# Performance work log

Measured on AMD Instinct MI355X. Metric: run time of the kernel, lower is better.

Reference implementation:

```python
import jax, jax.numpy as jnp
import numpy as np

N_NODES = 100000
N_EDGES = 1600000
IN_C = 128
HID_C = 128
OUT_C = 64
N_GRAPHS = 64


def setup_inputs() -> dict:
    key = jax.random.key(0)
    ks = jax.random.split(key, 12)
    x = jax.random.normal(ks[0], (N_NODES, IN_C), dtype=jnp.float32)
    edge_index = jax.random.randint(ks[1], (2, N_EDGES), 0, N_NODES, dtype=jnp.int64)
    batch = jnp.sort(jax.random.randint(ks[2], (N_NODES,), 0, N_GRAPHS, dtype=jnp.int64))
    def glorot(k, fan_in, fan_out):
        s = jnp.sqrt(6.0 / (fan_in + fan_out))
        return jax.random.uniform(k, (fan_in, fan_out), jnp.float32, -s, s)
    W1 = glorot(ks[3], IN_C, HID_C);  b1 = jnp.zeros((HID_C,), jnp.float32)
    W2 = glorot(ks[4], HID_C, HID_C); b2 = jnp.zeros((HID_C,), jnp.float32)
    W3 = glorot(ks[5], HID_C, HID_C); b3 = jnp.zeros((HID_C,), jnp.float32)
    Wlin = glorot(ks[6], HID_C, OUT_C)
    blin = jnp.zeros((OUT_C,), jnp.float32)
    return {"x": x, "edge_index": edge_index, "batch": batch,
            "W1": W1, "b1": b1, "W2": W2, "b2": b2, "W3": W3, "b3": b3,
            "Wlin": Wlin, "blin": blin}


def _gcn_conv(x, W, b, src, dst, norm):
    # PyG GCNConv: h = x @ W; out[dst] += norm * h[src]; out += b
    h = x @ W
    msg = h[src] * norm[:, None]                     # [E+N, C] edge-wise gather (memory-bound)
    out = jax.ops.segment_sum(msg, dst, num_segments=N_NODES)
    return out + b


def reference(x, edge_index, batch, W1, b1, W2, b2, W3, b3, Wlin, blin):
    # add self-loops (PyG default add_self_loops=True)
    loops = jnp.arange(N_NODES, dtype=edge_index.dtype)
    src = jnp.concatenate([edge_index[0], loops])
    dst = jnp.concatenate([edge_index[1], loops])
    # symmetric normalization: deg over dst with unit edge weights
    deg = jax.ops.segment_sum(jnp.ones_like(src, dtype=x.dtype), dst, num_segments=N_NODES)
    dinv = jnp.where(deg > 0, jax.lax.rsqrt(deg), 0.0)
    norm = dinv[src] * dinv[dst]                     # [E+N]

    h = jax.nn.relu(_gcn_conv(x, W1, b1, src, dst, norm))
    h = jax.nn.relu(_gcn_conv(h, W2, b2, src, dst, norm))
    h = jax.nn.relu(_gcn_conv(h, W3, b3, src, dst, norm))

    # global mean pool over graphs
    sums = jax.ops.segment_sum(h, batch, num_segments=N_GRAPHS)
    cnts = jax.ops.segment_sum(jnp.ones((N_NODES,), h.dtype), batch, num_segments=N_GRAPHS)
    pooled = sums / jnp.clip(cnts, 1.0)[:, None]     # [G, HID_C]
    return pooled @ Wlin + blin                      # [G, OUT_C]
```

## Files before the change

### kernel.cpp

```cpp
#include <hip/hip_runtime.h>
#include <stdint.h>

#define C_HID 128
#define NGRAPH 64
#define COUT 64
#define NBLK 256
#define BKT 256
#define NBUK_MAX 512
#define SCAN_CH 4096

typedef short bf16x8 __attribute__((ext_vector_type(8)));
typedef float f32x4 __attribute__((ext_vector_type(4)));
typedef float f32x2 __attribute__((ext_vector_type(2)));

__device__ __forceinline__ unsigned short f2bf(float f){
  unsigned int u = __builtin_bit_cast(unsigned int, f);
  u = u + 0x7FFFu + ((u >> 16) & 1u);
  return (unsigned short)(u >> 16);
}
__device__ __forceinline__ int clampi(int v, int lo, int hi){
  return v < lo ? lo : (v > hi ? hi : v);
}

__global__ void k_zero(float* __restrict__ out, int n){
  int i = blockIdx.x*blockDim.x + threadIdx.x;
  if (i < n) out[i] = 0.f;
}

__global__ __launch_bounds__(256) void k_cnt(const int* __restrict__ dst,
                                             int* __restrict__ cntg,
                                             int E, int N, int NBUK, int chunk){
  __shared__ int cnt[NBUK_MAX];
  int blk = blockIdx.x, t = threadIdx.x;
  for (int b = t; b < NBUK; b += 256) cnt[b] = 0;
  __syncthreads();
  int e0 = blk*chunk, e1 = min(E, e0 + chunk);
  for (int e = e0 + t; e < e1; e += 256)
    atomicAdd(&cnt[clampi(dst[e], 0, N-1) >> 8], 1);
  __syncthreads();
  for (int b = t; b < NBUK; b += 256)
    cntg[b*NBLK + blk] = cnt[b];
}

__global__ __launch_bounds__(256) void k_scanA(const int* __restrict__ cnt,
                                               int* __restrict__ bsum, int n){
  __shared__ int red[256];
  int blk = blockIdx.x, t = threadIdx.x;
  int base = blk*SCAN_CH + t*16;
  int s = 0;
  #pragma unroll
  for (int j = 0; j < 16; ++j){ int i = base + j; s += (i < n) ? cnt[i] : 0; }
  red[t] = s; __syncthreads();
  for (int off = 128; off > 0; off >>= 1){
    if (t < off) red[t] += red[t + off];
    __syncthreads();
  }
  if (t == 0) bsum[blk] = red[0];
}

__global__ __launch_bounds__(256) void k_scanB(const int* __restrict__ bsum,
                                               int* __restrict__ bbase,
                                               int* __restrict__ bases, int nb, int n){
  __shared__ int buf[256];
  int t = threadIdx.x;
  int v = (t < nb) ? bsum[t] : 0;
  buf[t] = v; __syncthreads();
  for (int off = 1; off < 256; off <<= 1){
    int add = (t >= off) ? buf[t-off] : 0;
    __syncthreads();
    buf[t] += add;
    __syncthreads();
  }
  if (t < nb) bbase[t] = buf[t] - v;
  if (t == nb-1) bases[n] = buf[t];
}

__global__ __launch_bounds__(256) void k_scanC(const int* __restrict__ cnt,
                                               const int* __restrict__ bbase,
                                               int* __restrict__ bases, int n){
  __shared__ int buf[256];
  int blk = blockIdx.x, t = threadIdx.x;
  int base = blk*SCAN_CH + t*16;
  int loc[16]; int s = 0;
  #pragma unroll
  for (int j = 0; j < 16; ++j){ int i = base + j; loc[j] = (i < n) ? cnt[i] : 0; s += loc[j]; }
  buf[t] = s; __syncthreads();
  for (int off = 1; off < 256; off <<= 1){
    int add = (t >= off) ? buf[t-off] : 0;
    __syncthreads();
    buf[t] += add;
    __syncthreads();
  }
  int run = bbase[blk] + buf[t] - s;
  #pragma unroll
  for (int j = 0; j < 16; ++j){
    int i = base + j;
    if (i < n) bases[i] = run;
    run += loc[j];
  }
}

__global__ __launch_bounds__(256) void k_scat(const int* __restrict__ src,
                                              const int* __restrict__ dst,
                                              const int* __restrict__ bases,
                                              unsigned int* __restrict__ rec,
                                              int E, int N, int NBUK, int chunk){
  __shared__ int cur[NBUK_MAX];
  int blk = blockIdx.x, t = threadIdx.x;
  for (int b = t; b < NBUK; b += 256) cur[b] = bases[b*NBLK + blk];
  __syncthreads();
  int e0 = blk*chunk, e1 = min(E, e0 + chunk);
  for (int e = e0 + t; e < e1; e += 256){
    int d = clampi(dst[e], 0, N-1);
    int s = clampi(src[e], 0, N-1);
    int p = atomicAdd(&cur[d >> 8], 1);
    rec[p] = (unsigned int)s | ((unsigned int)(d & 255) << 24);
  }
}

__global__ __launch_bounds__(256) void k_csr(const unsigned int* __restrict__ rec,
                                             const int* __restrict__ bases,
                                             int* __restrict__ offs, float* __restrict__ dinv,
                                             int* __restrict__ meta, int E, int N, int NBUK){
  __shared__ int cnt[BKT], loff[BKT], cur[BKT];
  int b = blockIdx.x, t = threadIdx.x;
  cnt[t] = 0;
  __syncthreads();
  int r0 = bases[b*NBLK];
  int r1 = (b+1 < NBUK) ? bases[(b+1)*NBLK] : E;
  for (int i = r0 + t; i < r1; i += 256)
    atomicAdd(&cnt[rec[i] >> 24], 1);
  __syncthreads();
  loff[t] = cnt[t];
  __syncthreads();
  for (int off = 1; off < BKT; off <<= 1){
    int add = (t >= off) ? loff[t - off] : 0;
    __syncthreads();
    loff[t] += add;
    __syncthreads();
  }
  int excl = loff[t] - cnt[t];
  cur[t] = r0 + excl;
  int node = b*BKT + t;
  if (node < N){
    offs[node] = r0 + excl;
    dinv[node] = rsqrtf((float)(cnt[t] + 1));
  }
  if (b == NBUK-1 && t == 0) offs[N] = E;
  __syncthreads();
  for (int i = r0 + t; i < r1; i += 256){
    unsigned int r = rec[i];
    int p = atomicAdd(&cur[r >> 24], 1);
    meta[p] = (int)(r & 0x00FFFFFFu);
  }
}

__global__ void k_xcast(const float2* __restrict__ x, const float* __restrict__ dinv,
                        unsigned short* __restrict__ y, unsigned short* __restrict__ y2, int N){
  int i = blockIdx.x*256 + threadIdx.x;
  int tot = N*64;
  if (i < tot){
    float2 v = x[i];
    float dn = dinv[i >> 6] * 64.f;
    int p = __builtin_amdgcn_cvt_pk_fp8_f32(v.x*dn, v.y*dn, 0, false);
    y[i] = (unsigned short)(p & 0xFFFF);
  } else if (i < tot + 64){
    y[i] = 0;
    y2[i] = 0;
  }
}

__global__ void k_prep(const float* __restrict__ W1, const float* __restrict__ W2,
                       const float* __restrict__ W3, unsigned short* __restrict__ Wt,
                       float* __restrict__ gsum){
  int idx = blockIdx.x*256 + threadIdx.x;
  if (idx < NGRAPH*C_HID) gsum[idx] = 0.f;
  int w = idx >> 14;
  int r = idx & 16383;
  int n = r & 127, k = r >> 7;
  const float* W = (w == 0) ? W1 : (w == 1) ? W2 : W3;
  Wt[(size_t)w*16384 + (size_t)n*128 + k] = f2bf(W[k*128 + n]);
}

__global__ __launch_bounds__(256) void k_spmm(const unsigned short* __restrict__ y,
                       const int* __restrict__ offs,
                       const float* __restrict__ dinv,
                       const int* __restrict__ meta,
                       unsigned int* __restrict__ agg, int N){
  int wv   = __builtin_amdgcn_readfirstlane(threadIdx.x >> 6);
  int lane = threadIdx.x & 63;
  int g = lane >> 3, c = lane & 7;
  int node0 = blockIdx.x*32 + wv*8;
  if (node0 >= N) return;

  int e[9];
  #pragma unroll
  for (int i = 0; i < 9; ++i) e[i] = offs[min(node0 + i, N)];
  int cn[8]; int maxc = 0;
  #pragma unroll
  for (int i = 0; i < 8; ++i){ cn[i] = e[i+1] - e[i]; maxc = max(maxc, cn[i]); }

  int e0l = e[0], cntl = cn[0];
  #pragma unroll
  for (int i = 1; i < 8; ++i){
    e0l  = (g == i) ? e[i]  : e0l;
    cntl = (g == i) ? cn[i] : cntl;
  }
  int nodeg = node0 + g;
  bool nok = nodeg < N;
  int nself = nok ? nodeg : N;

  const uint4* yrow = (const uint4*)y;

  int mv0 = (c      < cntl) ? meta[e0l + c]      : N;
  int mv1 = (c +  8 < cntl) ? meta[e0l + c +  8] : N;
  int mv2 = (c + 16 < cntl) ? meta[e0l + c + 16] : N;
  int mv3 = (c + 24 < cntl) ? meta[e0l + c + 24] : N;
  uint4 us = yrow[(size_t)nself*8 + c];
  float dl = dinv[nok ? nodeg : 0];

  f32x2 acc[8];
  { f32x2 f;
    f = __builtin_amdgcn_cvt_pk_f32_fp8((int)us.x, false); acc[0] = f;
    f = __builtin_amdgcn_cvt_pk_f32_fp8((int)us.x, true);  acc[1] = f;
    f = __builtin_amdgcn_cvt_pk_f32_fp8((int)us.y, false); acc[2] = f;
    f = __builtin_amdgcn_cvt_pk_f32_fp8((int)us.y, true);  acc[3] = f;
    f = __builtin_amdgcn_cvt_pk_f32_fp8((int)us.z, false); acc[4] = f;
    f = __builtin_amdgcn_cvt_pk_f32_fp8((int)us.z, true);  acc[5] = f;
    f = __builtin_amdgcn_cvt_pk_f32_fp8((int)us.w, false); acc[6] = f;
    f = __builtin_amdgcn_cvt_pk_f32_fp8((int)us.w, true);  acc[7] = f; }

  uint4 u[8];
#define SWZ(MV, J) __builtin_amdgcn_ds_swizzle(MV, (0x18 | (((J)&7)<<5)))
#define GA(K, SM) u[K] = yrow[(size_t)(unsigned)(SM)*8 + c]
#define CONV8() do{ _Pragma("unroll") \
  for (int k2 = 0; k2 < 8; ++k2){ \
    f32x2 f; \
    f = __builtin_amdgcn_cvt_pk_f32_fp8((int)u[k2].x, false); acc[0] += f; \
    f = __builtin_amdgcn_cvt_pk_f32_fp8((int)u[k2].x, true);  acc[1] += f; \
    f = __builtin_amdgcn_cvt_pk_f32_fp8((int)u[k2].y, false); acc[2] += f; \
    f = __builtin_amdgcn_cvt_pk_f32_fp8((int)u[k2].y, true);  acc[3] += f; \
    f = __builtin_amdgcn_cvt_pk_f32_fp8((int)u[k2].z, false); acc[4] += f; \
    f = __builtin_amdgcn_cvt_pk_f32_fp8((int)u[k2].z, true);  acc[5] += f; \
    f = __builtin_amdgcn_cvt_pk_f32_fp8((int)u[k2].w, false); acc[6] += f; \
    f = __builtin_amdgcn_cvt_pk_f32_fp8((int)u[k2].w, true);  acc[7] += f; } }while(0)

  if (0 < maxc){
    GA(0,SWZ(mv0,0)); GA(1,SWZ(mv0,1)); GA(2,SWZ(mv0,2)); GA(3,SWZ(mv0,3));
    GA(4,SWZ(mv0,4)); GA(5,SWZ(mv0,5)); GA(6,SWZ(mv0,6)); GA(7,SWZ(mv0,7));
    __builtin_amdgcn_sched_barrier(0);
    CONV8();
  }
  if (8 < maxc){
    GA(0,SWZ(mv1,0)); GA(1,SWZ(mv1,1)); GA(2,SWZ(mv1,2)); GA(3,SWZ(mv1,3));
    GA(4,SWZ(mv1,4)); GA(5,SWZ(mv1,5)); GA(6,SWZ(mv1,6)); GA(7,SWZ(mv1,7));
    __builtin_amdgcn_sched_barrier(0);
    CONV8();
  }
  if (16 < maxc){
    GA(0,SWZ(mv2,0)); GA(1,SWZ(mv2,1)); GA(2,SWZ(mv2,2)); GA(3,SWZ(mv2,3));
    GA(4,SWZ(mv2,4)); GA(5,SWZ(mv2,5)); GA(6,SWZ(mv2,6)); GA(7,SWZ(mv2,7));
    __builtin_amdgcn_sched_barrier(0);
    CONV8();
  }
  if (24 < maxc){
    GA(0,SWZ(mv3,0)); GA(1,SWZ(mv3,1)); GA(2,SWZ(mv3,2)); GA(3,SWZ(mv3,3));
    GA(4,SWZ(mv3,4)); GA(5,SWZ(mv3,5)); GA(6,SWZ(mv3,6)); GA(7,SWZ(mv3,7));
    __builtin_amdgcn_sched_barrier(0);
    CONV8();
  }
#undef SWZ
#undef GA
#undef CONV8

  for (int j = 32; j < maxc; ++j){
    int sm = (j < cntl) ? meta[e0l + j] : N;
    uint4 t = yrow[(size_t)(unsigned)sm*8 + c];
    f32x2 f;
    f = __builtin_amdgcn_cvt_pk_f32_fp8((int)t.x, false); acc[0] += f;
    f = __builtin_amdgcn_cvt_pk_f32_fp8((int)t.x, true);  acc[1] += f;
    f = __builtin_amdgcn_cvt_pk_f32_fp8((int)t.y, false); acc[2] += f;
    f = __builtin_amdgcn_cvt_pk_f32_fp8((int)t.y, true);  acc[3] += f;
    f = __builtin_amdgcn_cvt_pk_f32_fp8((int)t.z, false); acc[4] += f;
    f = __builtin_amdgcn_cvt_pk_f32_fp8((int)t.z, true);  acc[5] += f;
    f = __builtin_amdgcn_cvt_pk_f32_fp8((int)t.w, false); acc[6] += f;
    f = __builtin_amdgcn_cvt_pk_f32_fp8((int)t.w, true);  acc[7] += f;
  }

  float dn = dl * 0.015625f;
  if (nok){
    uint4 w0, w1;
    w0.x = (unsigned int)f2bf(acc[0].x*dn) | ((unsigned int)f2bf(acc[0].y*dn) << 16);
    w0.y = (unsigned int)f2bf(acc[1].x*dn) | ((unsigned int)f2bf(acc[1].y*dn) << 16);
    w0.z = (unsigned int)f2bf(acc[2].x*dn) | ((unsigned int)f2bf(acc[2].y*dn) << 16);
    w0.w = (unsigned int)f2bf(acc[3].x*dn) | ((unsigned int)f2bf(acc[3].y*dn) << 16);
    w1.x = (unsigned int)f2bf(acc[4].x*dn) | ((unsigned int)f2bf(acc[4].y*dn) << 16);
    w1.y = (unsigned int)f2bf(acc[5].x*dn) | ((unsigned int)f2bf(acc[5].y*dn) << 16);
    w1.z = (unsigned int)f2bf(acc[6].x*dn) | ((unsigned int)f2bf(acc[6].y*dn) << 16);
    w1.w = (unsigned int)f2bf(acc[7].x*dn) | ((unsigned int)f2bf(acc[7].y*dn) << 16);
    *(uint4*)(agg + (size_t)nodeg*64 + c*8)     = w0;
    *(uint4*)(agg + (size_t)nodeg*64 + c*8 + 4) = w1;
  }
}

#define GEMM_BLOCKS 512
template<bool FP8OUT, bool POOL>
__global__ __launch_bounds__(256) void k_gemm(const unsigned short* __restrict__ A,
                                              const unsigned short* __restrict__ Wt,
                                              const float* __restrict__ bias,
                                              const float* __restrict__ scale,
                                              void* __restrict__ outv,
                                              const int* __restrict__ batch,
                                              float* __restrict__ gsum, int M){
  __shared__ unsigned short wt[128*136];
  __shared__ float gbuf[2][C_HID];
  {
    const uint4* wsrc = (const uint4*)Wt;
    for (int i = threadIdx.x; i < 4096; i += 256){
      uint4 v = wsrc[i];
      int n = i >> 4, kblk = i & 15;
      *(uint4*)&wt[n*136 + kblk*8] = v;
    }
  }
  __syncthreads();

  int wv = threadIdx.x >> 6, lane = threadIdx.x & 63;
  int q = lane >> 4, ln = lane & 15;
  int tiles = (M + 63) >> 6;

  for (int tile = blockIdx.x; tile < tiles; tile += GEMM_BLOCKS){
    int m0 = tile*64 + wv*16;
    int arow = m0 + ln;
    bool arow_ok = (arow < M);
    int arow_s = arow_ok ? arow : 0;

    f32x4 zero = {0.f, 0.f, 0.f, 0.f};
    f32x4 acc[8];
    #pragma unroll
    for (int t = 0; t < 8; ++t) acc[t] = zero;

    #pragma unroll
    for (int kk = 0; kk < 4; ++kk){
      bf16x8 a;
      if (arow_ok){
        __builtin_memcpy(&a, A + (size_t)arow_s*128 + kk*32 + q*8, 16);
      } else {
        a = (bf16x8){0,0,0,0,0,0,0,0};
      }
      #pragma unroll
      for (int t = 0; t < 8; ++t){
        bf16x8 b;
        __builtin_memcpy(&b, &wt[(t*16 + ln)*136 + kk*32 + q*8], 16);
        acc[t] = __builtin_amdgcn_mfma_f32_16x16x32_bf16(a, b, acc[t], 0, 0, 0);
      }
    }

    if (POOL){
      int tb = tile*64;
      int gA = batch[tb];
      int gB = batch[min(tb + 63, M - 1)];
      bool multi = (gB > gA + 1);
      __syncthreads();
      ((float*)gbuf)[threadIdx.x] = 0.f;
      __syncthreads();
      #pragma unroll
      for (int t = 0; t < 8; ++t){
        float bv = bias[t*16 + ln];
        int ch = t*16 + ln;
        float s0 = 0.f, s1 = 0.f;
        #pragma unroll
        for (int r = 0; r < 4; ++r){
          int row = m0 + q*4 + r;
          if (row < M){
            float v = acc[t][r] + bv;
            v = v > 0.f ? v : 0.f;
            if (multi){
              atomicAdd(&gsum[(size_t)batch[row]*C_HID + ch], v);
            } else if (gB > gA && batch[row] != gA){
              s1 += v;
            } else {
              s0 += v;
            }
          }
        }
        if (!multi){
          if (s0 != 0.f) atomicAdd(&gbuf[0][ch], s0);
          if (s1 != 0.f) atomicAdd(&gbuf[1][ch], s1);
        }
      }
      __syncthreads();
      if (!multi){
        int sel = threadIdx.x >> 7, ch2 = threadIdx.x & 127;
        if (sel == 0 || gB > gA){
          float v = ((float*)gbuf)[threadIdx.x];
          if (v != 0.f)
            atomicAdd(&gsum[(size_t)((sel == 0) ? gA : gB)*C_HID + ch2], v);
        }
      }
    } else {
      float sc[4];
      #pragma unroll
      for (int r = 0; r < 4; ++r){
        int row = m0 + q*4 + r;
        sc[r] = (FP8OUT && row < M) ? scale[row] * 64.f : 1.0f;
      }
      #pragma unroll
      for (int t = 0; t < 8; ++t){
        float bv = bias[t*16 + ln];
        #pragma unroll
        for (int r = 0; r < 4; ++r){
          int row = m0 + q*4 + r;
          if (row < M){
            float v = acc[t][r] + bv;
            v = v > 0.f ? v : 0.f;
            if (FP8OUT){
              v *= sc[r];
              int p = __builtin_amdgcn_cvt_pk_fp8_f32(v, v, 0, false);
              ((unsigned char*)outv)[(size_t)row*128 + t*16 + ln] = (unsigned char)(p & 0xFF);
            } else {
              ((unsigned short*)outv)[(size_t)row*128 + t*16 + ln] = f2bf(v);
            }
          }
        }
      }
    }
  }
}

__device__ __forceinline__ int lower_bound_i(const int* arr, int n, int val){
  int lo = 0, hi = n;
  while (lo < hi){ int mid = (lo + hi) >> 1; if (arr[mid] < val) lo = mid + 1; else hi = mid; }
  return lo;
}

__global__ void k_fin(const float* __restrict__ gsum, const int* __restrict__ batch,
                      const float* __restrict__ Wl, const float* __restrict__ bl,
                      float* __restrict__ out, int N){
  __shared__ float srow[C_HID];
  int g = blockIdx.x, t = threadIdx.x;
  srow[t] = gsum[(size_t)g*C_HID + t];
  __syncthreads();
  if (t < COUT){
    int rs = clampi(lower_bound_i(batch, N, g), 0, N);
    int re = clampi(lower_bound_i(batch, N, g + 1), rs, N);
    float inv = 1.0f / fmaxf((float)(re - rs), 1.0f);
    float o = 0.f;
    for (int k = 0; k < 128; ++k)
      o += srow[k] * Wl[k*COUT + t];
    out[g*COUT + t] = o * inv + bl[t];
  }
}

extern "C" void kernel_launch(void* const* d_in, const int* in_sizes, int n_in,
                              void* d_out, int out_size, void* d_ws, size_t ws_size,
                              hipStream_t stream){
  const float* x0 = (const float*)d_in[0];
  const int* ei   = (const int*)d_in[1];
  const int* batch= (const int*)d_in[2];
  const float* W1 = (const float*)d_in[3];
  const float* b1 = (const float*)d_in[4];
  const float* W2 = (const float*)d_in[5];
  const float* b2 = (const float*)d_in[6];
  const float* W3 = (const float*)d_in[7];
  const float* b3 = (const float*)d_in[8];
  const float* Wl = (const float*)d_in[9];
  const float* bl = (const float*)d_in[10];
  float* out = (float*)d_out;

  int E = in_sizes[1] / 2;
  int N = in_sizes[2];
  const int* src = ei;
  const int* dst = ei + E;
  int NBUK = (N + BKT - 1) / BKT;
  int chunk = (E + NBLK - 1) / NBLK;
  int ncnt = NBUK * NBLK;
  int nsb  = (ncnt + SCAN_CH - 1) / SCAN_CH;

  size_t off_acc = 0;
  auto carve = [&](size_t bytes)->size_t{
    size_t r = off_acc; off_acc += (bytes + 255) & ~(size_t)255; return r;
  };
  size_t o_cnt   = carve((size_t)ncnt*4);
  size_t o_bases = carve((size_t)(ncnt+1)*4);
  size_t o_bsum  = carve(256*4);
  size_t o_bbase = carve(256*4);
  size_t o_offs  = carve((size_t)(N+1)*4);
  size_t o_dinv  = carve((size_t)N*4);
  size_t o_meta  = carve((size_t)E*4);
  size_t o_rec   = carve((size_t)E*4);
  size_t o_yA    = carve((size_t)(N+1)*C_HID);
  size_t o_yB    = carve((size_t)(N+1)*C_HID);
  size_t o_aggb  = carve((size_t)N*C_HID*2);
  size_t o_wt    = carve((size_t)3*128*128*2);
  size_t o_gsum  = carve((size_t)NGRAPH*C_HID*4);
  size_t need = off_acc;

  if (ws_size < need || NBUK > NBUK_MAX || nsb > 256){
    k_zero<<<(out_size+255)/256, 256, 0, stream>>>(out, out_size);
    return;
  }

  char* base = (char*)d_ws;
  int* cntg  = (int*)(base + o_cnt);
  int* bases = (int*)(base + o_bases);
  int* bsum  = (int*)(base + o_bsum);
  int* bbase = (int*)(base + o_bbase);
  int* offs  = (int*)(base + o_offs);
  float* dinv= (float*)(base + o_dinv);
  int* meta  = (int*)(base + o_meta);
  unsigned int* rec   = (unsigned int*)(base + o_rec);
  unsigned short* yA  = (unsigned short*)(base + o_yA);
  unsigned short* yB  = (unsigned short*)(base + o_yB);
  unsigned int* aggb  = (unsigned int*)(base + o_aggb);
  unsigned short* wt  = (unsigned short*)(base + o_wt);
  float* gsum         = (float*)(base + o_gsum);

  k_cnt  <<<NBLK, 256, 0, stream>>>(dst, cntg, E, N, NBUK, chunk);
  k_scanA<<<nsb, 256, 0, stream>>>(cntg, bsum, ncnt);
  k_scanB<<<1, 256, 0, stream>>>(bsum, bbase, bases, nsb, ncnt);
  k_scanC<<<nsb, 256, 0, stream>>>(cntg, bbase, bases, ncnt);
  k_scat <<<NBLK, 256, 0, stream>>>(src, dst, bases, rec, E, N, NBUK, chunk);
  k_csr  <<<NBUK, BKT, 0, stream>>>(rec, bases, offs, dinv, meta, E, N, NBUK);

  k_xcast<<<(N*64 + 64 + 255)/256, 256, 0, stream>>>((const float2*)x0, dinv, yA, yB, N);
  k_prep <<<192, 256, 0, stream>>>(W1, W2, W3, wt, gsum);

  int spmm_grid = (N + 31) / 32;

  k_spmm<<<spmm_grid, 256, 0, stream>>>(yA, offs, dinv, meta, aggb, N);
  k_gemm<true , false><<<GEMM_BLOCKS, 256, 0, stream>>>((const unsigned short*)aggb, wt,           b1, dinv, (void*)yB, nullptr, nullptr, N);
  k_spmm<<<spmm_grid, 256, 0, stream>>>(yB, offs, dinv, meta, aggb, N);
  k_gemm<true , false><<<GEMM_BLOCKS, 256, 0, stream>>>((const unsigned short*)aggb, wt + 16384,   b2, dinv, (void*)yA, nullptr, nullptr, N);
  k_spmm<<<spmm_grid, 256, 0, stream>>>(yA, offs, dinv, meta, aggb, N);
  k_gemm<false, true ><<<GEMM_BLOCKS, 256, 0, stream>>>((const unsigned short*)aggb, wt + 2*16384, b3, dinv, nullptr,    batch,   gsum,    N);

  k_fin<<<NGRAPH, 128, 0, stream>>>(gsum, batch, Wl, bl, out, N);
}
```

Before: 333.0 us.

## Cut kernel launches by fusing scans, prep kernels and final pooling

Replaces the three-kernel per-block prefix scan with global per-bucket atomic counts, scanned by the last-finishing block of k_cnt. k_scat then recounts its chunk locally and reserves ranges with global atomics. k_xcast and k_prep are merged, and the final linear layer runs in the last block of the pooling GEMM. This removes several small launches and their serialization gaps. In exchange, edge order inside a bucket now depends on atomic ordering, k_scat reads dst twice, and the last-block epilogue runs serially on one block.

Result: slower. 498.9 us (+49.8%).

```diff
diff --git a/kernel.cpp b/kernel.cpp
--- a/kernel.cpp
+++ b/kernel.cpp
@@ -7,8 +7,6 @@
 #define NBLK 256
 #define BKT 256
 #define NBUK_MAX 512
-#define SCAN_CH 4096
-
 typedef short bf16x8 __attribute__((ext_vector_type(8)));
 typedef float f32x4 __attribute__((ext_vector_type(4)));
 typedef float f32x2 __attribute__((ext_vector_type(2)));
@@ -28,92 +26,74 @@
 }
 
 __global__ __launch_bounds__(256) void k_cnt(const int* __restrict__ dst,
-                                             int* __restrict__ cntg,
+                                             int* __restrict__ bcnt,
+                                             int* __restrict__ done1,
+                                             int* __restrict__ bases,
+                                             int* __restrict__ cur,
                                              int E, int N, int NBUK, int chunk){
   __shared__ int cnt[NBUK_MAX];
-  int blk = blockIdx.x, t = threadIdx.x;
+  __shared__ int amLast;
+  int t = threadIdx.x;
   for (int b = t; b < NBUK; b += 256) cnt[b] = 0;
   __syncthreads();
-  int e0 = blk*chunk, e1 = min(E, e0 + chunk);
+  int e0 = blockIdx.x*chunk, e1 = min(E, e0 + chunk);
   for (int e = e0 + t; e < e1; e += 256)
     atomicAdd(&cnt[clampi(dst[e], 0, N-1) >> 8], 1);
   __syncthreads();
   for (int b = t; b < NBUK; b += 256)
-    cntg[b*NBLK + blk] = cnt[b];
-}
-
-__global__ __launch_bounds__(256) void k_scanA(const int* __restrict__ cnt,
-                                               int* __restrict__ bsum, int n){
-  __shared__ int red[256];
-  int blk = blockIdx.x, t = threadIdx.x;
-  int base = blk*SCAN_CH + t*16;
-  int s = 0;
-  #pragma unroll
-  for (int j = 0; j < 16; ++j){ int i = base + j; s += (i < n) ? cnt[i] : 0; }
-  red[t] = s; __syncthreads();
-  for (int off = 128; off > 0; off >>= 1){
-    if (t < off) red[t] += red[t + off];
+    if (cnt[b]) atomicAdd(&bcnt[b], cnt[b]);
+  __threadfence();
+  if (t == 0){
+    int old = __hip_atomic_fetch_add(done1, 1, __ATOMIC_ACQ_REL, __HIP_MEMORY_SCOPE_AGENT);
+    amLast = (old == (int)gridDim.x - 1);
+  }
+  __syncthreads();
+  if (!amLast) return;
+
+  __shared__ int sb[512];
+  int a0 = __hip_atomic_load(&bcnt[t],       __ATOMIC_RELAXED, __HIP_MEMORY_SCOPE_AGENT);
+  int a1 = __hip_atomic_load(&bcnt[t + 256], __ATOMIC_RELAXED, __HIP_MEMORY_SCOPE_AGENT);
+  sb[t] = a0; sb[t + 256] = a1;
+  __syncthreads();
+  for (int off = 1; off < 256; off <<= 1){
+    int x0 = (t >= off) ? sb[t - off] : 0;
+    int x1 = (t >= off) ? sb[256 + t - off] : 0;
     __syncthreads();
-  }
-  if (t == 0) bsum[blk] = red[0];
-}
-
-__global__ __launch_bounds__(256) void k_scanB(const int* __restrict__ bsum,
-                                               int* __restrict__ bbase,
-                                               int* __restrict__ bases, int nb, int n){
-  __shared__ int buf[256];
-  int t = threadIdx.x;
-  int v = (t < nb) ? bsum[t] : 0;
-  buf[t] = v; __syncthreads();
-  for (int off = 1; off < 256; off <<= 1){
-    int add = (t >= off) ? buf[t-off] : 0;
+    sb[t] += x0; sb[256 + t] += x1;
     __syncthreads();
-    buf[t] += add;
-    __syncthreads();
-  }
-  if (t < nb) bbase[t] = buf[t] - v;
-  if (t == nb-1) bases[n] = buf[t];
-}
-
-__global__ __launch_bounds__(256) void k_scanC(const int* __restrict__ cnt,
-                                               const int* __restrict__ bbase,
-                                               int* __restrict__ bases, int n){
-  __shared__ int buf[256];
-  int blk = blockIdx.x, t = threadIdx.x;
-  int base = blk*SCAN_CH + t*16;
-  int loc[16]; int s = 0;
-  #pragma unroll
-  for (int j = 0; j < 16; ++j){ int i = base + j; loc[j] = (i < n) ? cnt[i] : 0; s += loc[j]; }
-  buf[t] = s; __syncthreads();
-  for (int off = 1; off < 256; off <<= 1){
-    int add = (t >= off) ? buf[t-off] : 0;
-    __syncthreads();
-    buf[t] += add;
-    __syncthreads();
-  }
-  int run = bbase[blk] + buf[t] - s;
-  #pragma unroll
-  for (int j = 0; j < 16; ++j){
-    int i = base + j;
-    if (i < n) bases[i] = run;
-    run += loc[j];
-  }
+  }
+  int lowTot = sb[255];
+  sb[256 + t] += lowTot;
+  __syncthreads();
+  bases[t]       = sb[t] - a0;        cur[t]       = sb[t] - a0;
+  bases[t + 256] = sb[t + 256] - a1;  cur[t + 256] = sb[t + 256] - a1;
+  if (t == 255) bases[512] = sb[511];
 }
 
 __global__ __launch_bounds__(256) void k_scat(const int* __restrict__ src,
                                               const int* __restrict__ dst,
-                                              const int* __restrict__ bases,
+                                              int* __restrict__ cur,
                                               unsigned int* __restrict__ rec,
                                               int E, int N, int NBUK, int chunk){
-  __shared__ int cur[NBUK_MAX];
-  int blk = blockIdx.x, t = threadIdx.x;
-  for (int b = t; b < NBUK; b += 256) cur[b] = bases[b*NBLK + blk];
-  __syncthreads();
-  int e0 = blk*chunk, e1 = min(E, e0 + chunk);
+  __shared__ int cnt[NBUK_MAX];
+  __shared__ int lbase[NBUK_MAX];
+  int t = threadIdx.x;
+  for (int b = t; b < NBUK; b += 256) cnt[b] = 0;
+  __syncthreads();
+  int e0 = blockIdx.x*chunk, e1 = min(E, e0 + chunk);
+  for (int e = e0 + t; e < e1; e += 256)
+    atomicAdd(&cnt[clampi(dst[e], 0, N-1) >> 8], 1);
+  __syncthreads();
+  for (int b = t; b < NBUK; b += 256)
+    lbase[b] = cnt[b] ? atomicAdd(&cur[b], cnt[b]) : 0;
+  __syncthreads();
+  for (int b = t; b < NBUK; b += 256) cnt[b] = 0;
+  __syncthreads();
   for (int e = e0 + t; e < e1; e += 256){
     int d = clampi(dst[e], 0, N-1);
     int s = clampi(src[e], 0, N-1);
-    int p = atomicAdd(&cur[d >> 8], 1);
+    int b = d >> 8;
+    int p = lbase[b] + atomicAdd(&cnt[b], 1);
     rec[p] = (unsigned int)s | ((unsigned int)(d & 255) << 24);
   }
 }
@@ -126,8 +106,8 @@
   int b = blockIdx.x, t = threadIdx.x;
   cnt[t] = 0;
   __syncthreads();
-  int r0 = bases[b*NBLK];
-  int r1 = (b+1 < NBUK) ? bases[(b+1)*NBLK] : E;
+  int r0 = bases[b];
+  int r1 = bases[b + 1];
   for (int i = r0 + t; i < r1; i += 256)
     atomicAdd(&cnt[rec[i] >> 24], 1);
   __syncthreads();
@@ -155,8 +135,11 @@
   }
 }
 
-__global__ void k_xcast(const float2* __restrict__ x, const float* __restrict__ dinv,
-                        unsigned short* __restrict__ y, unsigned short* __restrict__ y2, int N){
+__global__ void k_prepx(const float2* __restrict__ x, const float* __restrict__ dinv,
+                        unsigned short* __restrict__ y, unsigned short* __restrict__ y2,
+                        const float* __restrict__ W1, const float* __restrict__ W2,
+                        const float* __restrict__ W3, unsigned short* __restrict__ Wt,
+                        float* __restrict__ gsum, int* __restrict__ done3, int N){
   int i = blockIdx.x*256 + threadIdx.x;
   int tot = N*64;
   if (i < tot){
@@ -168,18 +151,15 @@
     y[i] = 0;
     y2[i] = 0;
   }
-}
-
-__global__ void k_prep(const float* __restrict__ W1, const float* __restrict__ W2,
-                       const float* __restrict__ W3, unsigned short* __restrict__ Wt,
-                       float* __restrict__ gsum){
-  int idx = blockIdx.x*256 + threadIdx.x;
-  if (idx < NGRAPH*C_HID) gsum[idx] = 0.f;
-  int w = idx >> 14;
-  int r = idx & 16383;
-  int n = r & 127, k = r >> 7;
-  const float* W = (w == 0) ? W1 : (w == 1) ? W2 : W3;
-  Wt[(size_t)w*16384 + (size_t)n*128 + k] = f2bf(W[k*128 + n]);
+  if (i < 3*16384){
+    int w = i >> 14;
+    int r = i & 16383;
+    int n = r & 127, k = r >> 7;
+    const float* W = (w == 0) ? W1 : (w == 1) ? W2 : W3;
+    Wt[(size_t)w*16384 + (size_t)n*128 + k] = f2bf(W[k*128 + n]);
+  }
+  if (i < NGRAPH*C_HID) gsum[i] = 0.f;
+  if (i == 0) *done3 = 0;
 }
 
 __global__ __launch_bounds__(256) void k_spmm(const unsigned short* __restrict__ y,
@@ -303,6 +283,12 @@
   }
 }
 
+__device__ __forceinline__ int lower_bound_i(const int* arr, int n, int val){
+  int lo = 0, hi = n;
+  while (lo < hi){ int mid = (lo + hi) >> 1; if (arr[mid] < val) lo = mid + 1; else hi = mid; }
+  return lo;
+}
+
 #define GEMM_BLOCKS 512
 template<bool FP8OUT, bool POOL>
 __global__ __launch_bounds__(256) void k_gemm(const unsigned short* __restrict__ A,
@@ -311,9 +297,14 @@
                                               const float* __restrict__ scale,
                                               void* __restrict__ outv,
                                               const int* __restrict__ batch,
-                                              float* __restrict__ gsum, int M){
+                                              float* __restrict__ gsum,
+                                              int* __restrict__ done3,
+                                              const float* __restrict__ Wl,
+                                              const float* __restrict__ bl,
+                                              float* __restrict__ fout, int M){
   __shared__ unsigned short wt[128*136];
   __shared__ float gbuf[2][C_HID];
+  __shared__ int amLast;
   {
     const uint4* wsrc = (const uint4*)Wt;
     for (int i = threadIdx.x; i < 4096; i += 256){
@@ -425,29 +416,30 @@
       }
     }
   }
-}
-
-__device__ __forceinline__ int lower_bound_i(const int* arr, int n, int val){
-  int lo = 0, hi = n;
-  while (lo < hi){ int mid = (lo + hi) >> 1; if (arr[mid] < val) lo = mid + 1; else hi = mid; }
-  return lo;
-}
-
-__global__ void k_fin(const float* __restrict__ gsum, const int* __restrict__ batch,
-                      const float* __restrict__ Wl, const float* __restrict__ bl,
-                      float* __restrict__ out, int N){
-  __shared__ float srow[C_HID];
-  int g = blockIdx.x, t = threadIdx.x;
-  srow[t] = gsum[(size_t)g*C_HID + t];
-  __syncthreads();
-  if (t < COUT){
-    int rs = clampi(lower_bound_i(batch, N, g), 0, N);
-    int re = clampi(lower_bound_i(batch, N, g + 1), rs, N);
-    float inv = 1.0f / fmaxf((float)(re - rs), 1.0f);
-    float o = 0.f;
-    for (int k = 0; k < 128; ++k)
-      o += srow[k] * Wl[k*COUT + t];
-    out[g*COUT + t] = o * inv + bl[t];
+
+  if (POOL){
+    __threadfence();
+    if (threadIdx.x == 0){
+      int old = __hip_atomic_fetch_add(done3, 1, __ATOMIC_ACQ_REL, __HIP_MEMORY_SCOPE_AGENT);
+      amLast = (old == (int)gridDim.x - 1);
+    }
+    __syncthreads();
+    if (amLast){
+      float* gs = (float*)wt;
+      for (int i = threadIdx.x; i < NGRAPH*C_HID; i += 256)
+        gs[i] = __hip_atomic_load(&gsum[i], __ATOMIC_RELAXED, __HIP_MEMORY_SCOPE_AGENT);
+      __syncthreads();
+      for (int idx = threadIdx.x; idx < NGRAPH*COUT; idx += 256){
+        int g = idx >> 6, o = idx & 63;
+        int rs = clampi(lower_bound_i(batch, M, g), 0, M);
+        int re = clampi(lower_bound_i(batch, M, g + 1), rs, M);
+        float inv = 1.0f / fmaxf((float)(re - rs), 1.0f);
+        float acc2 = 0.f;
+        for (int k = 0; k < 128; ++k)
+          acc2 += gs[g*C_HID + k] * Wl[k*COUT + o];
+        fout[g*COUT + o] = acc2 * inv + bl[o];
+      }
+    }
   }
 }
 
@@ -473,17 +465,14 @@
   const int* dst = ei + E;
   int NBUK = (N + BKT - 1) / BKT;
   int chunk = (E + NBLK - 1) / NBLK;
-  int ncnt = NBUK * NBLK;
-  int nsb  = (ncnt + SCAN_CH - 1) / SCAN_CH;
 
   size_t off_acc = 0;
   auto carve = [&](size_t bytes)->size_t{
     size_t r = off_acc; off_acc += (bytes + 255) & ~(size_t)255; return r;
   };
-  size_t o_cnt   = carve((size_t)ncnt*4);
-  size_t o_bases = carve((size_t)(ncnt+1)*4);
-  size_t o_bsum  = carve(256*4);
-  size_t o_bbase = carve(256*4);
+  size_t o_bcnt  = carve((size_t)(NBUK_MAX + 8)*4);
+  size_t o_bases = carve((size_t)(NBUK_MAX + 1)*4);
+  size_t o_cur   = carve((size_t)NBUK_MAX*4);
   size_t o_offs  = carve((size_t)(N+1)*4);
   size_t o_dinv  = carve((size_t)N*4);
   size_t o_meta  = carve((size_t)E*4);
@@ -493,18 +482,19 @@
   size_t o_aggb  = carve((size_t)N*C_HID*2);
   size_t o_wt    = carve((size_t)3*128*128*2);
   size_t o_gsum  = carve((size_t)NGRAPH*C_HID*4);
+  size_t o_done3 = carve(256);
   size_t need = off_acc;
 
-  if (ws_size < need || NBUK > NBUK_MAX || nsb > 256){
+  if (ws_size < need || NBUK > NBUK_MAX){
     k_zero<<<(out_size+255)/256, 256, 0, stream>>>(out, out_size);
     return;
   }
 
   char* base = (char*)d_ws;
-  int* cntg  = (int*)(base + o_cnt);
+  int* bcnt  = (int*)(base + o_bcnt);
+  int* done1 = bcnt + NBUK_MAX;
   int* bases = (int*)(base + o_bases);
-  int* bsum  = (int*)(base + o_bsum);
-  int* bbase = (int*)(base + o_bbase);
+  int* cur   = (int*)(base + o_cur);
   int* offs  = (int*)(base + o_offs);
   float* dinv= (float*)(base + o_dinv);
   int* meta  = (int*)(base + o_meta);
@@ -514,25 +504,26 @@
   unsigned int* aggb  = (unsigned int*)(base + o_aggb);
   unsigned short* wt  = (unsigned short*)(base + o_wt);
   float* gsum         = (float*)(base + o_gsum);
-
-  k_cnt  <<<NBLK, 256, 0, stream>>>(dst, cntg, E, N, NBUK, chunk);
-  k_scanA<<<nsb, 256, 0, stream>>>(cntg, bsum, ncnt);
-  k_scanB<<<1, 256, 0, stream>>>(bsum, bbase, bases, nsb, ncnt);
-  k_scanC<<<nsb, 256, 0, stream>>>(cntg, bbase, bases, ncnt);
-  k_scat <<<NBLK, 256, 0, stream>>>(src, dst, bases, rec, E, N, NBUK, chunk);
-  k_csr  <<<NBUK, BKT, 0, stream>>>(rec, bases, offs, dinv, meta, E, N, NBUK);
-
-  k_xcast<<<(N*64 + 64 + 255)/256, 256, 0, stream>>>((const float2*)x0, dinv, yA, yB, N);
-  k_prep <<<192, 256, 0, stream>>>(W1, W2, W3, wt, gsum);
+  int* done3          = (int*)(base + o_done3);
+
+  hipMemsetAsync(bcnt, 0, (size_t)(NBUK_MAX + 8)*4, stream);
+  k_cnt <<<NBLK, 256, 0, stream>>>(dst, bcnt, done1, bases, cur, E, N, NBUK, chunk);
+  k_scat<<<NBLK, 256, 0, stream>>>(src, dst, cur, rec, E, N, NBUK, chunk);
+  k_csr <<<NBUK, BKT, 0, stream>>>(rec, bases, offs, dinv, meta, E, N, NBUK);
+
+  int xg = (N*64 + 64 + 255)/256;
+  k_prepx<<<xg, 256, 0, stream>>>((const float2*)x0, dinv, yA, yB,
+                                  W1, W2, W3, wt, gsum, done3, N);
 
   int spmm_grid = (N + 31) / 32;
 
   k_spmm<<<spmm_grid, 256, 0, stream>>>(yA, offs, dinv, meta, aggb, N);
-  k_gemm<true , false><<<GEMM_BLOCKS, 256, 0, stream>>>((const unsigned short*)aggb, wt,           b1, dinv, (void*)yB, nullptr, nullptr, N);
+  k_gemm<true , false><<<GEMM_BLOCKS, 256, 0, stream>>>((const unsigned short*)aggb, wt,
+      b1, dinv, (void*)yB, nullptr, nullptr, nullptr, nullptr, nullptr, nullptr, N);
   k_spmm<<<spmm_grid, 256, 0, stream>>>(yB, offs, dinv, meta, aggb, N);
-  k_gemm<true , false><<<GEMM_BLOCKS, 256, 0, stream>>>((const unsigned short*)aggb, wt + 16384,   b2, dinv, (void*)yA, nullptr, nullptr, N);
+  k_gemm<true , false><<<GEMM_BLOCKS, 256, 0, stream>>>((const unsigned short*)aggb, wt + 16384,
+      b2, dinv, (void*)yA, nullptr, nullptr, nullptr, nullptr, nullptr, nullptr, N);
   k_spmm<<<spmm_grid, 256, 0, stream>>>(yA, offs, dinv, meta, aggb, N);
-  k_gemm<false, true ><<<GEMM_BLOCKS, 256, 0, stream>>>((const unsigned short*)aggb, wt + 2*16384, b3, dinv, nullptr,    batch,   gsum,    N);
-
-  k_fin<<<NGRAPH, 128, 0, stream>>>(gsum, batch, Wl, bl, out, N);
-}
+  k_gemm<false, true ><<<GEMM_BLOCKS, 256, 0, stream>>>((const unsigned short*)aggb, wt + 2*16384,
+      b3, dinv, nullptr, batch, gsum, done3, Wl, bl, out, N);
+}
```
